# Kernel tuning notes

Hardware: AMD Instinct MI355X
Metric: run time of the kernel (lower is better)

## Reference

```python
import jax, jax.numpy as jnp
import numpy as np


def _dwconv(x, w, pad):
    # x: [B,C,H,W], w: [C,1,kh,kw] depthwise conv (groups=C), no bias
    return jax.lax.conv_general_dilated(
        x, w, window_strides=(1, 1), padding=[(pad, pad), (pad, pad)],
        dimension_numbers=('NCHW', 'OIHW', 'NCHW'),
        feature_group_count=x.shape[1])


def _omni_shift(x, alpha, cw1, cw3, cw5):
    # OmniShift training branch: alpha-weighted identity + 1x1 + 3x3 + 5x5 depthwise convs
    return (alpha[0] * x + alpha[1] * _dwconv(x, cw1, 0)
            + alpha[2] * _dwconv(x, cw3, 1) + alpha[3] * _dwconv(x, cw5, 2))


def _wkv(w_dec, u, k, v):
    # Numerically-stable RWKV-v4 WKV recurrence. w_dec,u: [D]; k,v: [B,T,D]
    kT = jnp.swapaxes(k, 0, 1)  # [T,B,D]
    vT = jnp.swapaxes(v, 0, 1)
    z = jnp.zeros_like(k[:, 0])
    init = (z, z, jnp.full_like(z, -1e38))  # (a, b, running max exponent)

    def step(carry, kv):
        a, b, pp = carry
        kt, vt = kv
        ww = u + kt
        p = jnp.maximum(pp, ww)
        e1 = jnp.exp(pp - p)
        e2 = jnp.exp(ww - p)
        out = (e1 * a + e2 * vt) / (e1 * b + e2)
        ww2 = pp + w_dec
        p2 = jnp.maximum(ww2, kt)
        f1 = jnp.exp(ww2 - p2)
        f2 = jnp.exp(kt - p2)
        return (f1 * a + f2 * vt, f1 * b + f2, p2), out

    _, out = jax.lax.scan(step, init, (kT, vT))
    return jnp.swapaxes(out, 0, 1)


def _forward(x, alpha, cw1, cw3, cw5, Wk, Wv, Wr, Wo, spatial_decay, spatial_first, h, w):
    B, T, C = x.shape
    xi = x.reshape(B, h, w, C).transpose(0, 3, 1, 2)  # b (h w) c -> b c h w
    xi = _omni_shift(xi, alpha, cw1, cw3, cw5)
    xf = xi.transpose(0, 2, 3, 1).reshape(B, T, C)    # b c h w -> b (h w) c
    k = jnp.einsum('btc,oc->bto', xf, Wk)
    v = jnp.einsum('btc,oc->bto', xf, Wv)
    r = jnp.einsum('btc,oc->bto', xf, Wr)
    sr = jax.nn.sigmoid(r)
    # 'b (h w) c -> b (w h) c' : W-major reordering for the second scan direction
    k1 = k.reshape(B, h, w, C).transpose(0, 2, 1, 3).reshape(B, T, C)
    v1 = v.reshape(B, h, w, C).transpose(0, 2, 1, 3).reshape(B, T, C)
    ks = jnp.concatenate([k, k1], axis=2)   # [B,T,2C]
    vs = jnp.concatenate([v, v1], axis=2)
    srs = jnp.concatenate([sr, sr], axis=2)
    w_dec = -jnp.exp(spatial_decay / T)  # WKV kernel applies w = -exp(w)
    u = spatial_first / T
    xs = _wkv(w_dec, u, ks, vs)
    xs = xs * srs
    return jnp.einsum('btd,cd->btc', xs, Wo)  # output Linear(2C -> C), no bias


def setup_inputs() -> dict:
    key = jax.random.key(0)
    ks = jax.random.split(key, 11)
    B, h, w, C = 8, 64, 64, 256
    T = h * w
    s = 0.02
    return {
        'x': jax.random.normal(ks[0], (B, T, C), jnp.float32),
        'alpha': jax.random.normal(ks[1], (4,), jnp.float32),
        'cw1': jax.random.normal(ks[2], (C, 1, 1, 1), jnp.float32) * s,
        'cw3': jax.random.normal(ks[3], (C, 1, 3, 3), jnp.float32) * s,
        'cw5': jax.random.normal(ks[4], (C, 1, 5, 5), jnp.float32) * s,
        'Wk': jax.random.normal(ks[5], (C, C), jnp.float32) * s,
        'Wv': jax.random.normal(ks[6], (C, C), jnp.float32) * s,
        'Wr': jax.random.normal(ks[7], (C, C), jnp.float32) * s,
        'Wo': jax.random.normal(ks[8], (C, 2 * C), jnp.float32) * s,
        'spatial_decay': jax.random.normal(ks[9], (2 * C,), jnp.float32),
        'spatial_first': jax.random.normal(ks[10], (2 * C,), jnp.float32),
        'h': h,
        'w': w,
    }


def reference(x, alpha, cw1, cw3, cw5, Wk, Wv, Wr, Wo, spatial_decay, spatial_first, h, w):
    return _forward(x, alpha, cw1, cw3, cw5, Wk, Wv, Wr, Wo, spatial_decay, spatial_first, h, w)
```

## Files before the change

### kernel.cpp

```cpp
#include <hip/hip_runtime.h>
#include <math.h>
#include <stdint.h>

#define TT 4096
#define HH 64
#define WW 64
#define CC 256
#define NCH 64
#define LCH 64

typedef __bf16 bf16x8 __attribute__((ext_vector_type(8)));
typedef float  f32x4  __attribute__((ext_vector_type(4)));

__device__ __forceinline__ unsigned short f2bf(float x) {
    uint32_t u = __float_as_uint(x);
    u = (u + 0x7fffu + ((u >> 16) & 1u)) >> 16;
    return (unsigned short)u;
}
__device__ __forceinline__ float bf2f(unsigned short h) {
    return __uint_as_float(((uint32_t)h) << 16);
}
__device__ __forceinline__ float fast_rcp(float x) {
    float r;
    asm("v_rcp_f32 %0, %1" : "=v"(r) : "v"(x));
    return r;
}

__global__ __launch_bounds__(256)
void prep_all(const float* __restrict__ alpha,
              const float* __restrict__ cw1,
              const float* __restrict__ cw3,
              const float* __restrict__ cw5,
              const float* __restrict__ Wk, const float* __restrict__ Wv,
              const float* __restrict__ Wr, const float* __restrict__ Wo,
              float* __restrict__ weff,
              unsigned short* __restrict__ W2k, unsigned short* __restrict__ W2v,
              unsigned short* __restrict__ W2r, unsigned short* __restrict__ Wo2,
              int do_wo) {
    int bid = blockIdx.x, c = threadIdx.x;
    if (bid < 25) {
        int k = bid;
        float a0 = alpha[0], a1 = alpha[1], a2 = alpha[2], a3 = alpha[3];
        float v = a3 * cw5[c * 25 + k];
        int ky = k / 5, kx = k % 5;
        if (ky >= 1 && ky <= 3 && kx >= 1 && kx <= 3)
            v += a2 * cw3[c * 9 + (ky - 1) * 3 + (kx - 1)];
        if (k == 12) v += a1 * cw1[c] + a0;
        weff[k * CC + c] = v;
    } else if (bid < 281) {
        int n = bid - 25;
        float a;
        unsigned short h;
        a = Wk[n * 256 + c]; h = f2bf(a); W2k[n * 512 + c] = h; W2k[n * 512 + 256 + c] = f2bf(a - bf2f(h));
        a = Wv[n * 256 + c]; h = f2bf(a); W2v[n * 512 + c] = h; W2v[n * 512 + 256 + c] = f2bf(a - bf2f(h));
        a = Wr[n * 256 + c]; h = f2bf(a); W2r[n * 512 + c] = h; W2r[n * 512 + 256 + c] = f2bf(a - bf2f(h));
    } else if (do_wo) {
        int n = bid - 281;
        float a = Wo[n * 512 + c];
        unsigned short h = f2bf(a);
        Wo2[n * 1024 + c] = h; Wo2[n * 1024 + 256 + c] = f2bf(a - bf2f(h));
        float b = Wo[n * 512 + 256 + c];
        unsigned short h2 = f2bf(b);
        Wo2[n * 1024 + 512 + c] = h2; Wo2[n * 1024 + 768 + c] = f2bf(b - bf2f(h2));
    }
}

__global__ __launch_bounds__(256)
void prep_wo(const float* __restrict__ Wo, unsigned short* __restrict__ Wo2) {
    int n = blockIdx.x, c = threadIdx.x;
    float a = Wo[n * 512 + c];
    unsigned short h = f2bf(a);
    Wo2[n * 1024 + c] = h; Wo2[n * 1024 + 256 + c] = f2bf(a - bf2f(h));
    float b = Wo[n * 512 + 256 + c];
    unsigned short h2 = f2bf(b);
    Wo2[n * 1024 + 512 + c] = h2; Wo2[n * 1024 + 768 + c] = f2bf(b - bf2f(h2));
}

__global__ __launch_bounds__(256)
void omni_conv(const float* __restrict__ x,
               const float* __restrict__ weff,
               unsigned short* __restrict__ A2) {
    int xx = blockIdx.x;
    int y0 = blockIdx.y * 32;
    int b  = blockIdx.z;
    int c  = threadIdx.x;
    const float* xb = x + (size_t)b * TT * CC + c;
    unsigned short* Ab = A2 + (size_t)b * TT * 512 + c;

    float wk[25];
    #pragma unroll
    for (int k = 0; k < 25; ++k) wk[k] = weff[k * CC + c];

    float win[5][5];
    #pragma unroll
    for (int i = 0; i < 4; ++i) {
        int yy = y0 - 2 + i;
        #pragma unroll
        for (int dx = 0; dx < 5; ++dx) {
            int xc = xx + dx - 2;
            win[i][dx] = (yy >= 0 && xc >= 0 && xc < WW)
                         ? xb[(size_t)(yy * WW + xc) * CC] : 0.f;
        }
    }
    #pragma unroll
    for (int i = 0; i < 32; ++i) {
        int y = y0 + i;
        int yy = y + 2;
        #pragma unroll
        for (int dx = 0; dx < 5; ++dx) {
            int xc = xx + dx - 2;
            win[4][dx] = (yy < HH && xc >= 0 && xc < WW)
                         ? xb[(size_t)(yy * WW + xc) * CC] : 0.f;
        }
        float acc = 0.f;
        #pragma unroll
        for (int r = 0; r < 5; ++r)
            #pragma unroll
            for (int dx = 0; dx < 5; ++dx)
                acc = fmaf(wk[r * 5 + dx], win[r][dx], acc);
        unsigned short h = f2bf(acc);
        size_t o = (size_t)(y * WW + xx) * 512;
        Ab[o] = h;
        Ab[o + 256] = f2bf(acc - bf2f(h));
        #pragma unroll
        for (int r = 0; r < 4; ++r)
            #pragma unroll
            for (int dx = 0; dx < 5; ++dx)
                win[r][dx] = win[r + 1][dx];
    }
}

template<int KIND>
__device__ __forceinline__ void mfma_core(const unsigned short* __restrict__ A0,
                                          const unsigned short* __restrict__ A1,
                                          const unsigned short* __restrict__ W2,
                                          float* __restrict__ C,
                                          int m_blk, int n_blk, bool act) {
    __shared__ __align__(16) unsigned short L[2][4][128 * 32];
    int tid = threadIdx.x;
    int w = tid >> 6, l = tid & 63;
    int q = l >> 4, rr = l & 15;
    int wm = (w & 1) * 64, wn = (w >> 1) * 64;
    int srw = w * 16 + (l >> 2);
    int ss  = l & 3;

    const int NCHK = (KIND == 0) ? 8 : 16;
    const int LDW  = (KIND == 0) ? 512 : 1024;

    f32x4 acc[4][4];
    #pragma unroll
    for (int i = 0; i < 4; ++i)
        #pragma unroll
        for (int j = 0; j < 4; ++j)
            acc[i][j] = (f32x4){0.f, 0.f, 0.f, 0.f};

    auto stage = [&](int cc, int buf) {
        const unsigned short* Ab;
        int ah, al, wh, wl;
        if (KIND == 0) {
            Ab = A0; ah = cc * 32; al = 256 + cc * 32;
            wh = cc * 32; wl = 256 + cc * 32;
        } else {
            int c8 = cc & 7;
            Ab = (cc < 8) ? A0 : A1;
            ah = c8 * 32; al = 256 + c8 * 32;
            wh = ((cc < 8) ? 0 : 512) + c8 * 32;
            wl = ((cc < 8) ? 256 : 768) + c8 * 32;
        }
        #pragma unroll
        for (int i = 0; i < 2; ++i) {
            int r = i * 64 + srw;
            int sl = (ss ^ ((r >> 1) & 3)) * 8;
            size_t arow = (size_t)(m_blk + r) * 512;
            size_t wrow = (size_t)(n_blk + r) * LDW;
            int db = (i * 64 + w * 16) * 32;
            __builtin_amdgcn_global_load_lds(
                (const __attribute__((address_space(1))) void*)(Ab + arow + ah + sl),
                (__attribute__((address_space(3))) void*)&L[buf][0][db], 16, 0, 0);
            __builtin_amdgcn_global_load_lds(
                (const __attribute__((address_space(1))) void*)(Ab + arow + al + sl),
                (__attribute__((address_space(3))) void*)&L[buf][1][db], 16, 0, 0);
            __builtin_amdgcn_global_load_lds(
                (const __attribute__((address_space(1))) void*)(W2 + wrow + wh + sl),
                (__attribute__((address_space(3))) void*)&L[buf][2][db], 16, 0, 0);
            __builtin_amdgcn_global_load_lds(
                (const __attribute__((address_space(1))) void*)(W2 + wrow + wl + sl),
                (__attribute__((address_space(3))) void*)&L[buf][3][db], 16, 0, 0);
        }
    };

    stage(0, 0);
    stage(1, 1);

    for (int cc = 0; cc < NCHK; ++cc) {
        int buf = cc & 1;
        if (cc + 1 < NCHK) {
            asm volatile("s_waitcnt vmcnt(8)" ::: "memory");
        } else {
            asm volatile("s_waitcnt vmcnt(0)" ::: "memory");
        }
        __builtin_amdgcn_s_barrier();

        bf16x8 ah4[4], al4[4], wh4[4], wl4[4];
        #pragma unroll
        for (int f = 0; f < 4; ++f) {
            int Ra = wm + f * 16 + rr;
            int sa = (q ^ ((Ra >> 1) & 3)) * 8;
            ah4[f] = *(const bf16x8*)&L[buf][0][Ra * 32 + sa];
            al4[f] = *(const bf16x8*)&L[buf][1][Ra * 32 + sa];
            int Rw = wn + f * 16 + rr;
            int sw2 = (q ^ ((Rw >> 1) & 3)) * 8;
            wh4[f] = *(const bf16x8*)&L[buf][2][Rw * 32 + sw2];
            wl4[f] = *(const bf16x8*)&L[buf][3][Rw * 32 + sw2];
        }
        __builtin_amdgcn_s_setprio(1);
        #pragma unroll
        for (int fm = 0; fm < 4; ++fm)
            #pragma unroll
            for (int fn = 0; fn < 4; ++fn)
                acc[fm][fn] = __builtin_amdgcn_mfma_f32_16x16x32_bf16(
                    ah4[fm], wh4[fn], acc[fm][fn], 0, 0, 0);
        #pragma unroll
        for (int fm = 0; fm < 4; ++fm)
            #pragma unroll
            for (int fn = 0; fn < 4; ++fn)
                acc[fm][fn] = __builtin_amdgcn_mfma_f32_16x16x32_bf16(
                    al4[fm], wh4[fn], acc[fm][fn], 0, 0, 0);
        #pragma unroll
        for (int fm = 0; fm < 4; ++fm)
            #pragma unroll
            for (int fn = 0; fn < 4; ++fn)
                acc[fm][fn] = __builtin_amdgcn_mfma_f32_16x16x32_bf16(
                    ah4[fm], wl4[fn], acc[fm][fn], 0, 0, 0);
        __builtin_amdgcn_s_setprio(0);

        __builtin_amdgcn_s_barrier();
        if (cc + 2 < NCHK) stage(cc + 2, buf);
    }

    #pragma unroll
    for (int fm = 0; fm < 4; ++fm)
        #pragma unroll
        for (int fn = 0; fn < 4; ++fn) {
            int col = n_blk + wn + fn * 16 + rr;
            int row0 = m_blk + wm + fm * 16 + q * 4;
            f32x4 v = acc[fm][fn];
            #pragma unroll
            for (int j = 0; j < 4; ++j) {
                float o = v[j];
                if (act) o = 1.f / (1.f + __expf(-o));
                C[(size_t)(row0 + j) * 256 + col] = o;
            }
        }
}

__global__ __launch_bounds__(256, 2)
void gemm_kvr_mfma(const unsigned short* __restrict__ A2,
                   const unsigned short* __restrict__ W2k,
                   const unsigned short* __restrict__ W2v,
                   const unsigned short* __restrict__ W2r,
                   float* __restrict__ kb, float* __restrict__ vb,
                   float* __restrict__ rb) {
    int id = blockIdx.x;
    int xcd = id & 7;
    int j = id >> 3;
    int v = j % 6;
    int mq = j / 6;
    int m_blk = (mq * 8 + xcd) * 128;
    int mat = v >> 1;
    int n_blk = (v & 1) * 128;
    const unsigned short* W2 = (mat == 0) ? W2k : (mat == 1) ? W2v : W2r;
    float* C = (mat == 0) ? kb : (mat == 1) ? vb : rb;
    mfma_core<0>(A2, A2, W2, C, m_blk, n_blk, mat == 2);
}

__global__ __launch_bounds__(256, 2)
void gemm_out_mfma(const unsigned short* __restrict__ xs0,
                   const unsigned short* __restrict__ xs1,
                   const unsigned short* __restrict__ Wo2,
                   float* __restrict__ out) {
    int id = blockIdx.x;
    int xcd = id & 7;
    int j = id >> 3;
    int v = j & 1;
    int mq = j >> 1;
    int m_blk = (mq * 8 + xcd) * 128;
    mfma_core<1>(xs0, xs1, Wo2, out, m_blk, v * 128, false);
}

__global__ __launch_bounds__(256)
void wkv_pass1(const float* __restrict__ kin, const float* __restrict__ vin,
               const float* __restrict__ sdecay,
               float* __restrict__ cs_a, float* __restrict__ cs_b,
               float* __restrict__ cs_p) {
    int chA = blockIdx.x, dir = blockIdx.y, bb = blockIdx.z, c = threadIdx.x;
    int chB = chA + NCH / 2;
    float wd = -expf(sdecay[dir * CC + c] * (1.f / TT));
    const float* kb = kin + (size_t)bb * TT * CC + c;
    const float* vb = vin + (size_t)bb * TT * CC + c;
    float aA = 0.f, bA = 0.f, pA = -1e38f;
    float aB = 0.f, bB = 0.f, pB = -1e38f;
    for (int i0 = 0; i0 < LCH; i0 += 8) {
        float kA8[8], vA8[8], kB8[8], vB8[8];
        #pragma unroll
        for (int i = 0; i < 8; ++i) {
            int ii = i0 + i;
            int sA = dir ? (ii * WW + chA) : (chA * LCH + ii);
            int sB = dir ? (ii * WW + chB) : (chB * LCH + ii);
            kA8[i] = kb[(size_t)sA * CC]; vA8[i] = vb[(size_t)sA * CC];
            kB8[i] = kb[(size_t)sB * CC]; vB8[i] = vb[(size_t)sB * CC];
        }
        #pragma unroll
        for (int i = 0; i < 8; ++i) {
            {
                float kt = kA8[i], vt = vA8[i];
                float ww2 = pA + wd;
                float p2 = fmaxf(ww2, kt);
                float f1 = __expf(ww2 - p2), f2 = __expf(kt - p2);
                aA = f1 * aA + f2 * vt; bA = f1 * bA + f2; pA = p2;
            }
            {
                float kt = kB8[i], vt = vB8[i];
                float ww2 = pB + wd;
                float p2 = fmaxf(ww2, kt);
                float f1 = __expf(ww2 - p2), f2 = __expf(kt - p2);
                aB = f1 * aB + f2 * vt; bB = f1 * bB + f2; pB = p2;
            }
        }
    }
    size_t base = (size_t)(bb * 2 + dir) * NCH * CC + c;
    size_t oA = base + (size_t)chA * CC, oB = base + (size_t)chB * CC;
    cs_a[oA] = aA; cs_b[oA] = bA; cs_p[oA] = pA;
    cs_a[oB] = aB; cs_b[oB] = bB; cs_p[oB] = pB;
}

__global__ __launch_bounds__(64)
void wkv_scan2(const float* __restrict__ sdecay,
               float* __restrict__ cs_a, float* __restrict__ cs_b,
               float* __restrict__ cs_p) {
    int c = blockIdx.x, dir = blockIdx.y, bb = blockIdx.z;
    int lane = threadIdx.x;
    float wd = -expf(sdecay[dir * CC + c] * (1.f / TT));
    float Ld = (float)LCH * wd;
    size_t o = (size_t)(bb * 2 + dir) * NCH * CC + (size_t)lane * CC + c;
    float a = cs_a[o], b = cs_b[o], p = cs_p[o];
    #pragma unroll
    for (int s = 0; s < 6; ++s) {
        int dlt = 1 << s;
        float xa = __shfl_up(a, dlt, 64);
        float xb = __shfl_up(b, dlt, 64);
        float xp = __shfl_up(p, dlt, 64);
        if (lane >= dlt) {
            float sh = xp + Ld * (float)dlt;
            float pn = fmaxf(sh, p);
            float e1 = __expf(sh - pn), e2 = __expf(p - pn);
            a = e1 * xa + e2 * a; b = e1 * xb + e2 * b; p = pn;
        }
    }
    float ea = __shfl_up(a, 1, 64);
    float eb = __shfl_up(b, 1, 64);
    float ep = __shfl_up(p, 1, 64);
    if (lane == 0) { ea = 0.f; eb = 0.f; ep = -1e38f; }
    cs_a[o] = ea; cs_b[o] = eb; cs_p[o] = ep;
}

__global__ __launch_bounds__(256)
void wkv_pass3(const float* __restrict__ kin, const float* __restrict__ vin,
               const float* __restrict__ srin,
               const float* __restrict__ sdecay, const float* __restrict__ sfirst,
               const float* __restrict__ cs_a, const float* __restrict__ cs_b,
               const float* __restrict__ cs_p,
               unsigned short* __restrict__ xs2_0, unsigned short* __restrict__ xs2_1) {
    int chA = blockIdx.x, dir = blockIdx.y, bb = blockIdx.z, c = threadIdx.x;
    int chB = chA + NCH / 2;
    int d = dir * CC + c;
    float u  = sfirst[d] * (1.f / TT);
    float wd = -expf(sdecay[d] * (1.f / TT));
    size_t base = (size_t)(bb * 2 + dir) * NCH * CC + c;
    size_t oA = base + (size_t)chA * CC, oB = base + (size_t)chB * CC;
    float aA = cs_a[oA], bA = cs_b[oA], pA = cs_p[oA];
    float aB = cs_a[oB], bB = cs_b[oB], pB = cs_p[oB];
    const float* kb  = kin  + (size_t)bb * TT * CC + c;
    const float* vb  = vin  + (size_t)bb * TT * CC + c;
    const float* srb = srin + (size_t)bb * TT * CC + c;
    unsigned short* xo = (dir ? xs2_1 : xs2_0) + (size_t)bb * TT * 512 + c;
    for (int i0 = 0; i0 < LCH; i0 += 8) {
        float kA8[8], vA8[8], sA8[8], kB8[8], vB8[8], sB8[8];
        #pragma unroll
        for (int i = 0; i < 8; ++i) {
            int ii = i0 + i;
            int tA = chA * LCH + ii;
            int tB = chB * LCH + ii;
            int sA = dir ? (ii * WW + chA) : tA;
            int sB = dir ? (ii * WW + chB) : tB;
            kA8[i] = kb[(size_t)sA * CC]; vA8[i] = vb[(size_t)sA * CC];
            sA8[i] = srb[(size_t)tA * CC];
            kB8[i] = kb[(size_t)sB * CC]; vB8[i] = vb[(size_t)sB * CC];
            sB8[i] = srb[(size_t)tB * CC];
        }
        #pragma unroll
        for (int i = 0; i < 8; ++i) {
            {
                int t = chA * LCH + i0 + i;
                float kt = kA8[i], vt = vA8[i];
                float ww = u + kt;
                float qq = fmaxf(pA, ww);
                float e1 = __expf(pA - qq), e2 = __expf(ww - qq);
                float num = e1 * aA + e2 * vt;
                float den = e1 * bA + e2;
                float os = num * fast_rcp(den) * sA8[i];
                unsigned short h = f2bf(os);
                xo[(size_t)t * 512] = h;
                xo[(size_t)t * 512 + 256] = f2bf(os - bf2f(h));
                float ww2 = pA + wd;
                float p2  = fmaxf(ww2, kt);
                float f1 = __expf(ww2 - p2), f2 = __expf(kt - p2);
                aA = f1 * aA + f2 * vt; bA = f1 * bA + f2; pA = p2;
            }
            {
                int t = chB * LCH + i0 + i;
                float kt = kB8[i], vt = vB8[i];
                float ww = u + kt;
                float qq = fmaxf(pB, ww);
                float e1 = __expf(pB - qq), e2 = __expf(ww - qq);
                float num = e1 * aB + e2 * vt;
                float den = e1 * bB + e2;
                float os = num * fast_rcp(den) * sB8[i];
                unsigned short h = f2bf(os);
                xo[(size_t)t * 512] = h;
                xo[(size_t)t * 512 + 256] = f2bf(os - bf2f(h));
                float ww2 = pB + wd;
                float p2  = fmaxf(ww2, kt);
                float f1 = __expf(ww2 - p2), f2 = __expf(kt - p2);
                aB = f1 * aB + f2 * vt; bB = f1 * bB + f2; pB = p2;
            }
        }
    }
}

extern "C" void kernel_launch(void* const* d_in, const int* in_sizes, int n_in,
                              void* d_out, int out_size, void* d_ws, size_t ws_size,
                              hipStream_t stream) {
    const float* x     = (const float*)d_in[0];
    const float* alpha = (const float*)d_in[1];
    const float* cw1   = (const float*)d_in[2];
    const float* cw3   = (const float*)d_in[3];
    const float* cw5   = (const float*)d_in[4];
    const float* Wk    = (const float*)d_in[5];
    const float* Wv    = (const float*)d_in[6];
    const float* Wr    = (const float*)d_in[7];
    const float* Wo    = (const float*)d_in[8];
    const float* sd    = (const float*)d_in[9];
    const float* sf    = (const float*)d_in[10];
    (void)n_in; (void)out_size;

    int B = in_sizes[0] / (TT * CC);
    int M = B * TT;
    size_t S = (size_t)M * 1024;

    char* wsb = (char*)d_ws;
    unsigned short* A2    = (unsigned short*)wsb;
    float*          kbuf  = (float*)(wsb + 1 * S);
    float*          vbuf  = (float*)(wsb + 2 * S);
    float*          srbuf = (float*)(wsb + 3 * S);
    unsigned short* xs2_1 = (unsigned short*)(wsb + 4 * S);
    unsigned short* xs2_0 = A2;

    bool wo_early = (ws_size >= 5 * S + 524288);
    unsigned short* Wo2 = wo_early ? (unsigned short*)(wsb + 5 * S)
                                   : (unsigned short*)(wsb + 3 * S);

    size_t SC = (size_t)B * 2 * NCH * CC;
    char* ob = (char*)d_out;
    float* cs_a = (float*)ob;
    float* cs_b = (float*)(ob + SC * 4);
    float* cs_p = (float*)(ob + 2 * SC * 4);
    float* weff = (float*)(ob + 3 * SC * 4);
    unsigned short* W2k = (unsigned short*)(ob + (4u << 20));
    unsigned short* W2v = (unsigned short*)(ob + (4u << 20) + 262144);
    unsigned short* W2r = (unsigned short*)(ob + (4u << 20) + 524288);

    prep_all<<<537, CC, 0, stream>>>(alpha, cw1, cw3, cw5, Wk, Wv, Wr, Wo,
                                     weff, W2k, W2v, W2r, Wo2,
                                     wo_early ? 1 : 0);
    omni_conv<<<dim3(WW, 2, B), CC, 0, stream>>>(x, weff, A2);

    gemm_kvr_mfma<<<(M / 128) * 6, 256, 0, stream>>>(A2, W2k, W2v, W2r,
                                                     kbuf, vbuf, srbuf);

    wkv_pass1<<<dim3(NCH / 2, 2, B), 256, 0, stream>>>(kbuf, vbuf, sd,
                                                       cs_a, cs_b, cs_p);
    wkv_scan2<<<dim3(CC, 2, B), 64, 0, stream>>>(sd, cs_a, cs_b, cs_p);
    wkv_pass3<<<dim3(NCH / 2, 2, B), 256, 0, stream>>>(kbuf, vbuf, srbuf, sd, sf,
                                                       cs_a, cs_b, cs_p,
                                                       xs2_0, xs2_1);

    if (!wo_early)
        prep_wo<<<256, CC, 0, stream>>>(Wo, Wo2);
    gemm_out_mfma<<<(M / 128) * 2, 256, 0, stream>>>(xs2_0, xs2_1, Wo2,
                                                     (float*)d_out);
}
```

Before: 283.0 us.

## Store k/v/r intermediates in bf16 and drop split-precision on WKV output

The k, v and sigmoid(r) GEMM outputs are now written as bf16 instead of fp32, halving the traffic of the WKV passes. The WKV output is stored as a single bf16 (no hi/lo split) into one interleaved buffer, so the output GEMM does two MFMA passes per chunk over fewer staged tiles instead of three. The chunk-carry scan is rewritten as a sequential per-channel loop, and the separate Wo prep kernel is removed by always preparing Wo in the first kernel with a re-laid-out Wo2. This trades accuracy in k/v/r and the output activations for less memory traffic and fewer MFMAs.

```diff
diff --git a/kernel.cpp b/kernel.cpp
--- a/kernel.cpp
+++ b/kernel.cpp
@@ -35,8 +35,7 @@
               const float* __restrict__ Wr, const float* __restrict__ Wo,
               float* __restrict__ weff,
               unsigned short* __restrict__ W2k, unsigned short* __restrict__ W2v,
-              unsigned short* __restrict__ W2r, unsigned short* __restrict__ Wo2,
-              int do_wo) {
+              unsigned short* __restrict__ W2r, unsigned short* __restrict__ Wo2) {
     int bid = blockIdx.x, c = threadIdx.x;
     if (bid < 25) {
         int k = bid;
@@ -54,26 +53,17 @@
         a = Wk[n * 256 + c]; h = f2bf(a); W2k[n * 512 + c] = h; W2k[n * 512 + 256 + c] = f2bf(a - bf2f(h));
         a = Wv[n * 256 + c]; h = f2bf(a); W2v[n * 512 + c] = h; W2v[n * 512 + 256 + c] = f2bf(a - bf2f(h));
         a = Wr[n * 256 + c]; h = f2bf(a); W2r[n * 512 + c] = h; W2r[n * 512 + 256 + c] = f2bf(a - bf2f(h));
-    } else if (do_wo) {
+    } else {
         int n = bid - 281;
         float a = Wo[n * 512 + c];
         unsigned short h = f2bf(a);
-        Wo2[n * 1024 + c] = h; Wo2[n * 1024 + 256 + c] = f2bf(a - bf2f(h));
+        Wo2[n * 1024 + c] = h;
+        Wo2[n * 1024 + 512 + c] = f2bf(a - bf2f(h));
         float b = Wo[n * 512 + 256 + c];
         unsigned short h2 = f2bf(b);
-        Wo2[n * 1024 + 512 + c] = h2; Wo2[n * 1024 + 768 + c] = f2bf(b - bf2f(h2));
-    }
-}
-
-__global__ __launch_bounds__(256)
-void prep_wo(const float* __restrict__ Wo, unsigned short* __restrict__ Wo2) {
-    int n = blockIdx.x, c = threadIdx.x;
-    float a = Wo[n * 512 + c];
-    unsigned short h = f2bf(a);
-    Wo2[n * 1024 + c] = h; Wo2[n * 1024 + 256 + c] = f2bf(a - bf2f(h));
-    float b = Wo[n * 512 + 256 + c];
-    unsigned short h2 = f2bf(b);
-    Wo2[n * 1024 + 512 + c] = h2; Wo2[n * 1024 + 768 + c] = f2bf(b - bf2f(h2));
+        Wo2[n * 1024 + 256 + c] = h2;
+        Wo2[n * 1024 + 512 + 256 + c] = f2bf(b - bf2f(h2));
+    }
 }
 
 __global__ __launch_bounds__(256)
@@ -132,11 +122,11 @@
 
 template<int KIND>
 __device__ __forceinline__ void mfma_core(const unsigned short* __restrict__ A0,
-                                          const unsigned short* __restrict__ A1,
                                           const unsigned short* __restrict__ W2,
-                                          float* __restrict__ C,
+                                          void* __restrict__ Cv,
                                           int m_blk, int n_blk, bool act) {
-    __shared__ __align__(16) unsigned short L[2][4][128 * 32];
+    constexpr int NT = (KIND == 0) ? 4 : 3;
+    __shared__ __align__(16) unsigned short L[2][NT][128 * 32];
     int tid = threadIdx.x;
     int w = tid >> 6, l = tid & 63;
     int q = l >> 4, rr = l & 15;
@@ -145,6 +135,7 @@
     int ss  = l & 3;
 
     const int NCHK = (KIND == 0) ? 8 : 16;
+    const int LDA  = 512;
     const int LDW  = (KIND == 0) ? 512 : 1024;
 
     f32x4 acc[4][4];
@@ -155,37 +146,38 @@
             acc[i][j] = (f32x4){0.f, 0.f, 0.f, 0.f};
 
     auto stage = [&](int cc, int buf) {
-        const unsigned short* Ab;
-        int ah, al, wh, wl;
-        if (KIND == 0) {
-            Ab = A0; ah = cc * 32; al = 256 + cc * 32;
-            wh = cc * 32; wl = 256 + cc * 32;
-        } else {
-            int c8 = cc & 7;
-            Ab = (cc < 8) ? A0 : A1;
-            ah = c8 * 32; al = 256 + c8 * 32;
-            wh = ((cc < 8) ? 0 : 512) + c8 * 32;
-            wl = ((cc < 8) ? 256 : 768) + c8 * 32;
-        }
         #pragma unroll
         for (int i = 0; i < 2; ++i) {
             int r = i * 64 + srw;
             int sl = (ss ^ ((r >> 1) & 3)) * 8;
-            size_t arow = (size_t)(m_blk + r) * 512;
+            size_t arow = (size_t)(m_blk + r) * LDA;
             size_t wrow = (size_t)(n_blk + r) * LDW;
             int db = (i * 64 + w * 16) * 32;
-            __builtin_amdgcn_global_load_lds(
-                (const __attribute__((address_space(1))) void*)(Ab + arow + ah + sl),
-                (__attribute__((address_space(3))) void*)&L[buf][0][db], 16, 0, 0);
-            __builtin_amdgcn_global_load_lds(
-                (const __attribute__((address_space(1))) void*)(Ab + arow + al + sl),
-                (__attribute__((address_space(3))) void*)&L[buf][1][db], 16, 0, 0);
-            __builtin_amdgcn_global_load_lds(
-                (const __attribute__((address_space(1))) void*)(W2 + wrow + wh + sl),
-                (__attribute__((address_space(3))) void*)&L[buf][2][db], 16, 0, 0);
-            __builtin_amdgcn_global_load_lds(
-                (const __attribute__((address_space(1))) void*)(W2 + wrow + wl + sl),
-                (__attribute__((address_space(3))) void*)&L[buf][3][db], 16, 0, 0);
+            if (KIND == 0) {
+                int ah = cc * 32, al = 256 + cc * 32;
+                __builtin_amdgcn_global_load_lds(
+                    (const __attribute__((address_space(1))) void*)(A0 + arow + ah + sl),
+                    (__attribute__((address_space(3))) void*)&L[buf][0][db], 16, 0, 0);
+                __builtin_amdgcn_global_load_lds(
+                    (const __attribute__((address_space(1))) void*)(A0 + arow + al + sl),
+                    (__attribute__((address_space(3))) void*)&L[buf][1][db], 16, 0, 0);
+                __builtin_amdgcn_global_load_lds(
+                    (const __attribute__((address_space(1))) void*)(W2 + wrow + cc * 32 + sl),
+                    (__attribute__((address_space(3))) void*)&L[buf][2][db], 16, 0, 0);
+                __builtin_amdgcn_global_load_lds(
+                    (const __attribute__((address_space(1))) void*)(W2 + wrow + 256 + cc * 32 + sl),
+                    (__attribute__((address_space(3))) void*)&L[buf][3][db], 16, 0, 0);
+            } else {
+                __builtin_amdgcn_global_load_lds(
+                    (const __attribute__((address_space(1))) void*)(A0 + arow + cc * 32 + sl),
+                    (__attribute__((address_space(3))) void*)&L[buf][0][db], 16, 0, 0);
+                __builtin_amdgcn_global_load_lds(
+                    (const __attribute__((address_space(1))) void*)(W2 + wrow + cc * 32 + sl),
+                    (__attribute__((address_space(3))) void*)&L[buf][1][db], 16, 0, 0);
+                __builtin_amdgcn_global_load_lds(
+                    (const __attribute__((address_space(1))) void*)(W2 + wrow + 512 + cc * 32 + sl),
+                    (__attribute__((address_space(3))) void*)&L[buf][2][db], 16, 0, 0);
+            }
         }
     };
 
@@ -195,44 +187,73 @@
     for (int cc = 0; cc < NCHK; ++cc) {
         int buf = cc & 1;
         if (cc + 1 < NCHK) {
-            asm volatile("s_waitcnt vmcnt(8)" ::: "memory");
+            if (KIND == 0) asm volatile("s_waitcnt vmcnt(8)" ::: "memory");
+            else           asm volatile("s_waitcnt vmcnt(6)" ::: "memory");
         } else {
             asm volatile("s_waitcnt vmcnt(0)" ::: "memory");
         }
         __builtin_amdgcn_s_barrier();
 
-        bf16x8 ah4[4], al4[4], wh4[4], wl4[4];
-        #pragma unroll
-        for (int f = 0; f < 4; ++f) {
-            int Ra = wm + f * 16 + rr;
-            int sa = (q ^ ((Ra >> 1) & 3)) * 8;
-            ah4[f] = *(const bf16x8*)&L[buf][0][Ra * 32 + sa];
-            al4[f] = *(const bf16x8*)&L[buf][1][Ra * 32 + sa];
-            int Rw = wn + f * 16 + rr;
-            int sw2 = (q ^ ((Rw >> 1) & 3)) * 8;
-            wh4[f] = *(const bf16x8*)&L[buf][2][Rw * 32 + sw2];
-            wl4[f] = *(const bf16x8*)&L[buf][3][Rw * 32 + sw2];
-        }
-        __builtin_amdgcn_s_setprio(1);
-        #pragma unroll
-        for (int fm = 0; fm < 4; ++fm)
-            #pragma unroll
-            for (int fn = 0; fn < 4; ++fn)
-                acc[fm][fn] = __builtin_amdgcn_mfma_f32_16x16x32_bf16(
-                    ah4[fm], wh4[fn], acc[fm][fn], 0, 0, 0);
-        #pragma unroll
-        for (int fm = 0; fm < 4; ++fm)
-            #pragma unroll
-            for (int fn = 0; fn < 4; ++fn)
-                acc[fm][fn] = __builtin_amdgcn_mfma_f32_16x16x32_bf16(
-                    al4[fm], wh4[fn], acc[fm][fn], 0, 0, 0);
-        #pragma unroll
-        for (int fm = 0; fm < 4; ++fm)
-            #pragma unroll
-            for (int fn = 0; fn < 4; ++fn)
-                acc[fm][fn] = __builtin_amdgcn_mfma_f32_16x16x32_bf16(
-                    ah4[fm], wl4[fn], acc[fm][fn], 0, 0, 0);
-        __builtin_amdgcn_s_setprio(0);
+        if (KIND == 0) {
+            bf16x8 ah4[4], al4[4], wh4[4], wl4[4];
+            #pragma unroll
+            for (int f = 0; f < 4; ++f) {
+                int Ra = wm + f * 16 + rr;
+                int sa = (q ^ ((Ra >> 1) & 3)) * 8;
+                ah4[f] = *(const bf16x8*)&L[buf][0][Ra * 32 + sa];
+                al4[f] = *(const bf16x8*)&L[buf][1][Ra * 32 + sa];
+                int Rw = wn + f * 16 + rr;
+                int sw2 = (q ^ ((Rw >> 1) & 3)) * 8;
+                wh4[f] = *(const bf16x8*)&L[buf][2][Rw * 32 + sw2];
+                wl4[f] = *(const bf16x8*)&L[buf][3][Rw * 32 + sw2];
+            }
+            __builtin_amdgcn_s_setprio(1);
+            #pragma unroll
+            for (int fm = 0; fm < 4; ++fm)
+                #pragma unroll
+                for (int fn = 0; fn < 4; ++fn)
+                    acc[fm][fn] = __builtin_amdgcn_mfma_f32_16x16x32_bf16(
+                        ah4[fm], wh4[fn], acc[fm][fn], 0, 0, 0);
+            #pragma unroll
+            for (int fm = 0; fm < 4; ++fm)
+                #pragma unroll
+                for (int fn = 0; fn < 4; ++fn)
+                    acc[fm][fn] = __builtin_amdgcn_mfma_f32_16x16x32_bf16(
+                        al4[fm], wh4[fn], acc[fm][fn], 0, 0, 0);
+            #pragma unroll
+            for (int fm = 0; fm < 4; ++fm)
+                #pragma unroll
+                for (int fn = 0; fn < 4; ++fn)
+                    acc[fm][fn] = __builtin_amdgcn_mfma_f32_16x16x32_bf16(
+                        ah4[fm], wl4[fn], acc[fm][fn], 0, 0, 0);
+            __builtin_amdgcn_s_setprio(0);
+        } else {
+            bf16x8 a4[4], wh4[4], wl4[4];
+            #pragma unroll
+            for (int f = 0; f < 4; ++f) {
+                int Ra = wm + f * 16 + rr;
+                int sa = (q ^ ((Ra >> 1) & 3)) * 8;
+                a4[f] = *(const bf16x8*)&L[buf][0][Ra * 32 + sa];
+                int Rw = wn + f * 16 + rr;
+                int sw2 = (q ^ ((Rw >> 1) & 3)) * 8;
+                wh4[f] = *(const bf16x8*)&L[buf][1][Rw * 32 + sw2];
+                wl4[f] = *(const bf16x8*)&L[buf][2][Rw * 32 + sw2];
+            }
+            __builtin_amdgcn_s_setprio(1);
+            #pragma unroll
+            for (int fm = 0; fm < 4; ++fm)
+                #pragma unroll
+                for (int fn = 0; fn < 4; ++fn)
+                    acc[fm][fn] = __builtin_amdgcn_mfma_f32_16x16x32_bf16(
+                        a4[fm], wh4[fn], acc[fm][fn], 0, 0, 0);
+            #pragma unroll
+            for (int fm = 0; fm < 4; ++fm)
+                #pragma unroll
+                for (int fn = 0; fn < 4; ++fn)
+                    acc[fm][fn] = __builtin_amdgcn_mfma_f32_16x16x32_bf16(
+                        a4[fm], wl4[fn], acc[fm][fn], 0, 0, 0);
+            __builtin_amdgcn_s_setprio(0);
+        }
 
         __builtin_amdgcn_s_barrier();
         if (cc + 2 < NCHK) stage(cc + 2, buf);
@@ -248,8 +269,12 @@
             #pragma unroll
             for (int j = 0; j < 4; ++j) {
                 float o = v[j];
-                if (act) o = 1.f / (1.f + __expf(-o));
-                C[(size_t)(row0 + j) * 256 + col] = o;
+                if (KIND == 0) {
+                    if (act) o = 1.f / (1.f + __expf(-o));
+                    ((unsigned short*)Cv)[(size_t)(row0 + j) * 256 + col] = f2bf(o);
+                } else {
+                    ((float*)Cv)[(size_t)(row0 + j) * 256 + col] = o;
+                }
             }
         }
 }
@@ -259,8 +284,8 @@
                    const unsigned short* __restrict__ W2k,
                    const unsigned short* __restrict__ W2v,
                    const unsigned short* __restrict__ W2r,
-                   float* __restrict__ kb, float* __restrict__ vb,
-                   float* __restrict__ rb) {
+                   unsigned short* __restrict__ kb, unsigned short* __restrict__ vb,
+                   unsigned short* __restrict__ rb) {
     int id = blockIdx.x;
     int xcd = id & 7;
     int j = id >> 3;
@@ -270,13 +295,12 @@
     int mat = v >> 1;
     int n_blk = (v & 1) * 128;
     const unsigned short* W2 = (mat == 0) ? W2k : (mat == 1) ? W2v : W2r;
-    float* C = (mat == 0) ? kb : (mat == 1) ? vb : rb;
-    mfma_core<0>(A2, A2, W2, C, m_blk, n_blk, mat == 2);
+    unsigned short* C = (mat == 0) ? kb : (mat == 1) ? vb : rb;
+    mfma_core<0>(A2, W2, C, m_blk, n_blk, mat == 2);
 }
 
 __global__ __launch_bounds__(256, 2)
-void gemm_out_mfma(const unsigned short* __restrict__ xs0,
-                   const unsigned short* __restrict__ xs1,
+void gemm_out_mfma(const unsigned short* __restrict__ xs_all,
                    const unsigned short* __restrict__ Wo2,
                    float* __restrict__ out) {
     int id = blockIdx.x;
@@ -285,19 +309,20 @@
     int v = j & 1;
     int mq = j >> 1;
     int m_blk = (mq * 8 + xcd) * 128;
-    mfma_core<1>(xs0, xs1, Wo2, out, m_blk, v * 128, false);
+    mfma_core<1>(xs_all, Wo2, out, m_blk, v * 128, false);
 }
 
 __global__ __launch_bounds__(256)
-void wkv_pass1(const float* __restrict__ kin, const float* __restrict__ vin,
+void wkv_pass1(const unsigned short* __restrict__ kin,
+               const unsigned short* __restrict__ vin,
                const float* __restrict__ sdecay,
                float* __restrict__ cs_a, float* __restrict__ cs_b,
                float* __restrict__ cs_p) {
     int chA = blockIdx.x, dir = blockIdx.y, bb = blockIdx.z, c = threadIdx.x;
     int chB = chA + NCH / 2;
     float wd = -expf(sdecay[dir * CC + c] * (1.f / TT));
-    const float* kb = kin + (size_t)bb * TT * CC + c;
-    const float* vb = vin + (size_t)bb * TT * CC + c;
+    const unsigned short* kb = kin + (size_t)bb * TT * CC + c;
+    const unsigned short* vb = vin + (size_t)bb * TT * CC + c;
     float aA = 0.f, bA = 0.f, pA = -1e38f;
     float aB = 0.f, bB = 0.f, pB = -1e38f;
     for (int i0 = 0; i0 < LCH; i0 += 8) {
@@ -307,8 +332,8 @@
             int ii = i0 + i;
             int sA = dir ? (ii * WW + chA) : (chA * LCH + ii);
             int sB = dir ? (ii * WW + chB) : (chB * LCH + ii);
-            kA8[i] = kb[(size_t)sA * CC]; vA8[i] = vb[(size_t)sA * CC];
-            kB8[i] = kb[(size_t)sB * CC]; vB8[i] = vb[(size_t)sB * CC];
+            kA8[i] = bf2f(kb[(size_t)sA * CC]); vA8[i] = bf2f(vb[(size_t)sA * CC]);
+            kB8[i] = bf2f(kb[(size_t)sB * CC]); vB8[i] = bf2f(vb[(size_t)sB * CC]);
         }
         #pragma unroll
         for (int i = 0; i < 8; ++i) {
@@ -334,43 +359,34 @@
     cs_a[oB] = aB; cs_b[oB] = bB; cs_p[oB] = pB;
 }
 
-__global__ __launch_bounds__(64)
-void wkv_scan2(const float* __restrict__ sdecay,
+__global__ __launch_bounds__(256)
+void wkv_pass2(const float* __restrict__ sdecay,
                float* __restrict__ cs_a, float* __restrict__ cs_b,
                float* __restrict__ cs_p) {
-    int c = blockIdx.x, dir = blockIdx.y, bb = blockIdx.z;
-    int lane = threadIdx.x;
+    int bb = blockIdx.x, dir = blockIdx.y, c = threadIdx.x;
     float wd = -expf(sdecay[dir * CC + c] * (1.f / TT));
     float Ld = (float)LCH * wd;
-    size_t o = (size_t)(bb * 2 + dir) * NCH * CC + (size_t)lane * CC + c;
-    float a = cs_a[o], b = cs_b[o], p = cs_p[o];
-    #pragma unroll
-    for (int s = 0; s < 6; ++s) {
-        int dlt = 1 << s;
-        float xa = __shfl_up(a, dlt, 64);
-        float xb = __shfl_up(b, dlt, 64);
-        float xp = __shfl_up(p, dlt, 64);
-        if (lane >= dlt) {
-            float sh = xp + Ld * (float)dlt;
-            float pn = fmaxf(sh, p);
-            float e1 = __expf(sh - pn), e2 = __expf(p - pn);
-            a = e1 * xa + e2 * a; b = e1 * xb + e2 * b; p = pn;
-        }
-    }
-    float ea = __shfl_up(a, 1, 64);
-    float eb = __shfl_up(b, 1, 64);
-    float ep = __shfl_up(p, 1, 64);
-    if (lane == 0) { ea = 0.f; eb = 0.f; ep = -1e38f; }
-    cs_a[o] = ea; cs_b[o] = eb; cs_p[o] = ep;
+    float a = 0.f, b = 0.f, p = -1e38f;
+    size_t base = (size_t)(bb * 2 + dir) * NCH * CC + c;
+    for (int ch = 0; ch < NCH; ++ch) {
+        size_t o = base + (size_t)ch * CC;
+        float al = cs_a[o], bl = cs_b[o], pl = cs_p[o];
+        cs_a[o] = a; cs_b[o] = b; cs_p[o] = p;
+        float sh = p + Ld;
+        float pn = fmaxf(sh, pl);
+        float e1 = __expf(sh - pn), e2 = __expf(pl - pn);
+        a = e1 * a + e2 * al; b = e1 * b + e2 * bl; p = pn;
+    }
 }
 
 __global__ __launch_bounds__(256)
-void wkv_pass3(const float* __restrict__ kin, const float* __restrict__ vin,
-               const float* __restrict__ srin,
+void wkv_pass3(const unsigned short* __restrict__ kin,
+               const unsigned short* __restrict__ vin,
+               const unsigned short* __restrict__ srin,
                const float* __restrict__ sdecay, const float* __restrict__ sfirst,
                const float* __restrict__ cs_a, const float* __restrict__ cs_b,
                const float* __restrict__ cs_p,
-               unsigned short* __restrict__ xs2_0, unsigned short* __restrict__ xs2_1) {
+               unsigned short* __restrict__ xs_all) {
     int chA = blockIdx.x, dir = blockIdx.y, bb = blockIdx.z, c = threadIdx.x;
     int chB = chA + NCH / 2;
     int d = dir * CC + c;
@@ -380,10 +396,10 @@
     size_t oA = base + (size_t)chA * CC, oB = base + (size_t)chB * CC;
     float aA = cs_a[oA], bA = cs_b[oA], pA = cs_p[oA];
     float aB = cs_a[oB], bB = cs_b[oB], pB = cs_p[oB];
-    const float* kb  = kin  + (size_t)bb * TT * CC + c;
-    const float* vb  = vin  + (size_t)bb * TT * CC + c;
-    const float* srb = srin + (size_t)bb * TT * CC + c;
-    unsigned short* xo = (dir ? xs2_1 : xs2_0) + (size_t)bb * TT * 512 + c;
+    const unsigned short* kb  = kin  + (size_t)bb * TT * CC + c;
+    const unsigned short* vb  = vin  + (size_t)bb * TT * CC + c;
+    const unsigned short* srb = srin + (size_t)bb * TT * CC + c;
+    unsigned short* xo = xs_all + (size_t)bb * TT * 512 + dir * 256 + c;
     for (int i0 = 0; i0 < LCH; i0 += 8) {
         float kA8[8], vA8[8], sA8[8], kB8[8], vB8[8], sB8[8];
         #pragma unroll
@@ -393,10 +409,10 @@
             int tB = chB * LCH + ii;
             int sA = dir ? (ii * WW + chA) : tA;
             int sB = dir ? (ii * WW + chB) : tB;
-            kA8[i] = kb[(size_t)sA * CC]; vA8[i] = vb[(size_t)sA * CC];
-            sA8[i] = srb[(size_t)tA * CC];
-            kB8[i] = kb[(size_t)sB * CC]; vB8[i] = vb[(size_t)sB * CC];
-            sB8[i] = srb[(size_t)tB * CC];
+            kA8[i] = bf2f(kb[(size_t)sA * CC]); vA8[i] = bf2f(vb[(size_t)sA * CC]);
+            sA8[i] = bf2f(srb[(size_t)tA * CC]);
+            kB8[i] = bf2f(kb[(size_t)sB * CC]); vB8[i] = bf2f(vb[(size_t)sB * CC]);
+            sB8[i] = bf2f(srb[(size_t)tB * CC]);
         }
         #pragma unroll
         for (int i = 0; i < 8; ++i) {
@@ -409,9 +425,7 @@
                 float num = e1 * aA + e2 * vt;
                 float den = e1 * bA + e2;
                 float os = num * fast_rcp(den) * sA8[i];
-                unsigned short h = f2bf(os);
-                xo[(size_t)t * 512] = h;
-                xo[(size_t)t * 512 + 256] = f2bf(os - bf2f(h));
+                xo[(size_t)t * 512] = f2bf(os);
                 float ww2 = pA + wd;
                 float p2  = fmaxf(ww2, kt);
                 float f1 = __expf(ww2 - p2), f2 = __expf(kt - p2);
@@ -426,9 +440,7 @@
                 float num = e1 * aB + e2 * vt;
                 float den = e1 * bB + e2;
                 float os = num * fast_rcp(den) * sB8[i];
-                unsigned short h = f2bf(os);
-                xo[(size_t)t * 512] = h;
-                xo[(size_t)t * 512 + 256] = f2bf(os - bf2f(h));
+                xo[(size_t)t * 512] = f2bf(os);
                 float ww2 = pB + wd;
                 float p2  = fmaxf(ww2, kt);
                 float f1 = __expf(ww2 - p2), f2 = __expf(kt - p2);
@@ -452,23 +464,19 @@
     const float* Wo    = (const float*)d_in[8];
     const float* sd    = (const float*)d_in[9];
     const float* sf    = (const float*)d_in[10];
-    (void)n_in; (void)out_size;
+    (void)n_in; (void)out_size; (void)ws_size;
 
     int B = in_sizes[0] / (TT * CC);
     int M = B * TT;
     size_t S = (size_t)M * 1024;
 
     char* wsb = (char*)d_ws;
-    unsigned short* A2    = (unsigned short*)wsb;
-    float*          kbuf  = (float*)(wsb + 1 * S);
-    float*          vbuf  = (float*)(wsb + 2 * S);
-    float*          srbuf = (float*)(wsb + 3 * S);
-    unsigned short* xs2_1 = (unsigned short*)(wsb + 4 * S);
-    unsigned short* xs2_0 = A2;
-
-    bool wo_early = (ws_size >= 5 * S + 524288);
-    unsigned short* Wo2 = wo_early ? (unsigned short*)(wsb + 5 * S)
-                                   : (unsigned short*)(wsb + 3 * S);
+    unsigned short* A2     = (unsigned short*)wsb;
+    unsigned short* xs_all = A2;
+    unsigned short* kbuf   = (unsigned short*)(wsb + 1 * S);
+    unsigned short* vbuf   = (unsigned short*)(wsb + 1 * S + S / 2);
+    unsigned short* srbuf  = (unsigned short*)(wsb + 2 * S);
+    unsigned short* Wo2    = (unsigned short*)(wsb + 2 * S + S / 2);
 
     size_t SC = (size_t)B * 2 * NCH * CC;
     char* ob = (char*)d_out;
@@ -481,8 +489,7 @@
     unsigned short* W2r = (unsigned short*)(ob + (4u << 20) + 524288);
 
     prep_all<<<537, CC, 0, stream>>>(alpha, cw1, cw3, cw5, Wk, Wv, Wr, Wo,
-                                     weff, W2k, W2v, W2r, Wo2,
-                                     wo_early ? 1 : 0);
+                                     weff, W2k, W2v, W2r, Wo2);
     omni_conv<<<dim3(WW, 2, B), CC, 0, stream>>>(x, weff, A2);
 
     gemm_kvr_mfma<<<(M / 128) * 6, 256, 0, stream>>>(A2, W2k, W2v, W2r,
@@ -490,13 +497,9 @@
 
     wkv_pass1<<<dim3(NCH / 2, 2, B), 256, 0, stream>>>(kbuf, vbuf, sd,
                                                        cs_a, cs_b, cs_p);
-    wkv_scan2<<<dim3(CC, 2, B), 64, 0, stream>>>(sd, cs_a, cs_b, cs_p);
+    wkv_pass2<<<dim3(B, 2), 256, 0, stream>>>(sd, cs_a, cs_b, cs_p);
     wkv_pass3<<<dim3(NCH / 2, 2, B), 256, 0, stream>>>(kbuf, vbuf, srbuf, sd, sf,
-                                                       cs_a, cs_b, cs_p,
-                                                       xs2_0, xs2_1);
-
-    if (!wo_early)
-        prep_wo<<<256, CC, 0, stream>>>(Wo, Wo2);
-    gemm_out_mfma<<<(M / 128) * 2, 256, 0, stream>>>(xs2_0, xs2_1, Wo2,
-                                                     (float*)d_out);
-}
+                                                       cs_a, cs_b, cs_p, xs_all);
+
+    gemm_out_mfma<<<(M / 128) * 2, 256, 0, stream>>>(xs_all, Wo2, (float*)d_out);
+}
```

After: 243.3 us. 14.0% less time.
